# Kernel optimization log

Measured on AMD Instinct MI355X. Metric: run time of the kernel, lower is better.

## Reference

```python
import jax, jax.numpy as jnp
import numpy as np
import math

N_WAY, K_SHOT, Q_QUERY, PRJ_NUM, D = 5, 5, 15, 6, 64


def setup_inputs() -> dict:
    key = jax.random.key(0)
    k1, k2 = jax.random.split(key)
    feat = jax.random.normal(k1, (600, 64, 10, 10), dtype=jnp.float32)
    label = jax.random.randint(k2, (450,), 0, N_WAY)
    scale = jnp.ones((1,), dtype=jnp.float32)
    r = jnp.zeros((2,), dtype=jnp.float32)
    return {"feat": feat, "label": label, "scale": scale, "r": r}


def reference(feat, label, scale, r):
    ns = N_WAY * K_SHOT * PRJ_NUM  # 150 support images
    inv_sqrt_d = 1.0 / math.sqrt(D)
    support_xf = feat[:ns] * inv_sqrt_d
    query_xf = feat[ns:] * inv_sqrt_d
    q, c, h, w = query_xf.shape

    # support: (n_way, k_shot*prj_num*h*w, c)
    support = support_xf.reshape(N_WAY, K_SHOT * PRJ_NUM, c, h * w)
    support = jnp.transpose(support, (0, 1, 3, 2)).reshape(N_WAY, -1, c)
    # query: (q*h*w, c)
    query = jnp.transpose(query_xf.reshape(q, c, h * w), (0, 2, 1)).reshape(q * h * w, c)

    alpha, beta = r[0], r[1]
    reg = support.shape[1] / support.shape[2]
    lam = reg * jnp.exp(alpha)
    rho = jnp.exp(beta)

    # Woodbury / normal-equations path: hat = (S^T S + lam I)^-1 S^T S, per class
    sts = jnp.einsum('nkc,nkd->ncd', support, support)  # (n_way, c, c)
    m = sts + lam * jnp.eye(c, dtype=sts.dtype)[None]
    hat = jnp.linalg.inv(m) @ sts  # (n_way, c, c)

    Q_bar = jnp.einsum('qc,ncd->nqd', query, hat) * rho  # (n_way, q*h*w, c)
    dist = jnp.sum((Q_bar - query[None]) ** 2, axis=2).T  # (q*h*w, n_way)
    neg_l2_dist = -dist.reshape(q, h * w, N_WAY).mean(axis=1)  # (q, n_way)

    y_pred = jax.nn.softmax(neg_l2_dist, axis=1)
    logits = neg_l2_dist * scale[0]
    logp = jax.nn.log_softmax(logits, axis=1)
    loss = -jnp.mean(jnp.take_along_axis(logp, label[:, None], axis=1))
    return y_pred, loss
```

## Files before the change

kernel.cpp:

```cpp
#include <hip/hip_runtime.h>
#include <math.h>


typedef __attribute__((ext_vector_type(8))) short short8;
typedef __attribute__((ext_vector_type(4))) short short4v;
typedef __attribute__((ext_vector_type(4))) float f32x4;

#define NSUP 150
#define NQ 450
#define PIX 100
#define IMG_STRIDE 6400
#define MAGIC 0x5F3D2B1Cu

static __device__ __forceinline__ short bf16r(float x) {
  unsigned u = __builtin_bit_cast(unsigned, x);
  u += 0x7FFFu + ((u >> 16) & 1u);
  return (short)(u >> 16);
}
static __device__ __forceinline__ float b2f(short v) {
  return __builtin_bit_cast(float, ((unsigned)(unsigned short)v) << 16);
}
static __device__ __forceinline__ void st_flag(unsigned* p, unsigned v) {
  __threadfence();
  __hip_atomic_store(p, v, __ATOMIC_RELEASE, __HIP_MEMORY_SCOPE_AGENT);
}
static __device__ __forceinline__ void spin_flag(unsigned* p) {
  int guard = 1 << 22;
  while (__hip_atomic_load(p, __ATOMIC_ACQUIRE, __HIP_MEMORY_SCOPE_AGENT) != MAGIC
         && --guard) __builtin_amdgcn_s_sleep(2);
}

static __device__ __forceinline__ void gram_accum(const float* __restrict__ f,
                                                  f32x4 acc[4][4], int r, int g) {
  #pragma unroll
  for (int ks = 0; ks < 4; ++ks) {
    short8 frag[4];
    const int kb = ks * 32 + g * 8;
    #pragma unroll
    for (int R = 0; R < 4; ++R) {
      short8 q;
      const float* p = f + (R * 16 + r) * PIX + kb;
      if (ks < 3) {
        float4 lo = *(const float4*)p;
        float4 hi = *(const float4*)(p + 4);
        q[0] = bf16r(lo.x); q[1] = bf16r(lo.y); q[2] = bf16r(lo.z); q[3] = bf16r(lo.w);
        q[4] = bf16r(hi.x); q[5] = bf16r(hi.y); q[6] = bf16r(hi.z); q[7] = bf16r(hi.w);
      } else if (g == 0) {
        float4 lo = *(const float4*)p;
        q[0] = bf16r(lo.x); q[1] = bf16r(lo.y); q[2] = bf16r(lo.z); q[3] = bf16r(lo.w);
        q[4] = 0; q[5] = 0; q[6] = 0; q[7] = 0;
      } else {
        #pragma unroll
        for (int j = 0; j < 8; ++j) q[j] = 0;
      }
      frag[R] = q;
    }
    #pragma unroll
    for (int R = 0; R < 4; ++R)
      #pragma unroll
      for (int C = 0; C < 4; ++C)
        acc[R][C] = __builtin_amdgcn_mfma_f32_16x16x32_bf16(frag[R], frag[C],
                                                            acc[R][C], 0, 0, 0);
  }
}

static __device__ __forceinline__ void mm64q(const short* A, const short* B,
                                             f32x4 t[2][2], int r, int g,
                                             int wr, int wc) {
  #pragma unroll
  for (int ks = 0; ks < 2; ++ks) {
    short8 af[2], bfr[2];
    #pragma unroll
    for (int i = 0; i < 2; ++i) {
      af[i]  = *(const short8*)(A + (wr * 32 + i * 16 + r) * 72 + ks * 32 + g * 8);
      bfr[i] = *(const short8*)(B + (wc * 32 + i * 16 + r) * 72 + ks * 32 + g * 8);
    }
    #pragma unroll
    for (int i = 0; i < 2; ++i)
      #pragma unroll
      for (int j = 0; j < 2; ++j)
        t[i][j] = __builtin_amdgcn_mfma_f32_16x16x32_bf16(af[i], bfr[j],
                                                          t[i][j], 0, 0, 0);
  }
}

#define ZERO_ACC4(t)                                  \
  _Pragma("unroll") for (int R = 0; R < 4; ++R)       \
  _Pragma("unroll") for (int C = 0; C < 4; ++C)       \
  _Pragma("unroll") for (int q = 0; q < 4; ++q) t[R][C][q] = 0.f;

#define ZERO_ACC2(t)                                  \
  _Pragma("unroll") for (int R = 0; R < 2; ++R)       \
  _Pragma("unroll") for (int C = 0; C < 2; ++C)       \
  _Pragma("unroll") for (int q = 0; q < 4; ++q) t[R][C][q] = 0.f;

__global__ __launch_bounds__(256) void k_fused(
    const float* __restrict__ feat, const int* __restrict__ label,
    const float* __restrict__ scale, const float* __restrict__ rvec,
    float* __restrict__ out,
    float* __restrict__ partial,
    unsigned short* __restrict__ Gneg,
    float* __restrict__ blockloss,
    unsigned* __restrict__ gflag,
    unsigned* __restrict__ sflag,
    unsigned* __restrict__ lflag) {
  __shared__ __align__(16) char smem[65536];
  const int b = blockIdx.x, tid = threadIdx.x;
  const int wave = tid >> 6, lane = tid & 63;
  const int r = lane & 15, g = lane >> 4;

  if (b < 30) {
    float (*gbuf)[4096] = (float (*)[4096])smem;
    const int cls = b / 6, jb = b % 6;
    const int ks = wave, kb = ks * 32 + g * 8;
    f32x4 acc[4][4];
    ZERO_ACC4(acc)
    for (int im = 0; im < 5; ++im) {
      const float* f = feat + (size_t)(cls * 30 + jb * 5 + im) * IMG_STRIDE;
      short8 frag[4];
      #pragma unroll
      for (int R = 0; R < 4; ++R) {
        short8 q;
        const float* p = f + (R * 16 + r) * PIX + kb;
        if (ks < 3) {
          float4 lo = *(const float4*)p;
          float4 hi = *(const float4*)(p + 4);
          q[0] = bf16r(lo.x); q[1] = bf16r(lo.y); q[2] = bf16r(lo.z); q[3] = bf16r(lo.w);
          q[4] = bf16r(hi.x); q[5] = bf16r(hi.y); q[6] = bf16r(hi.z); q[7] = bf16r(hi.w);
        } else if (g == 0) {
          float4 lo = *(const float4*)p;
          q[0] = bf16r(lo.x); q[1] = bf16r(lo.y); q[2] = bf16r(lo.z); q[3] = bf16r(lo.w);
          q[4] = 0; q[5] = 0; q[6] = 0; q[7] = 0;
        } else {
          #pragma unroll
          for (int j = 0; j < 8; ++j) q[j] = 0;
        }
        frag[R] = q;
      }
      #pragma unroll
      for (int R = 0; R < 4; ++R)
        #pragma unroll
        for (int C = 0; C < 4; ++C)
          acc[R][C] = __builtin_amdgcn_mfma_f32_16x16x32_bf16(frag[R], frag[C],
                                                              acc[R][C], 0, 0, 0);
    }
    #pragma unroll
    for (int R = 0; R < 4; ++R)
      #pragma unroll
      for (int C = 0; C < 4; ++C)
        #pragma unroll
        for (int q = 0; q < 4; ++q) {
          const int row = R * 16 + g * 4 + q, col = C * 16 + r;
          gbuf[wave][row * 64 + col] = acc[R][C][q];
        }
    __syncthreads();
    float* outp = partial + (size_t)b * 4096;
    for (int c = tid; c < 1024; c += 256) {
      f32x4 s0 = *(const f32x4*)&gbuf[0][4 * c];
      f32x4 s1 = *(const f32x4*)&gbuf[1][4 * c];
      f32x4 s2 = *(const f32x4*)&gbuf[2][4 * c];
      f32x4 s3 = *(const f32x4*)&gbuf[3][4 * c];
      f32x4 s = s0 + s1 + s2 + s3;
      *(float4*)(outp + 4 * c) = *(float4*)&s;
    }
    __syncthreads();
    if (tid == 0) st_flag(&gflag[b], MAGIC);
    if (b >= 5) return;

    float* Ms   = (float*)(smem);
    short* Mb   = (short*)(smem + 16640);
    short* Tb   = (short*)(smem + 25856);
    short* Xa   = (short*)(smem + 35072);
    short* Xc   = (short*)(smem + 44288);
    float* radp = (float*)(smem + 53504);
    float* scal = (float*)(smem + 54528);

    const int n = b;
    const int wr = wave >> 1, wc = wave & 1;
    const float lam = 46.875f * expf(rvec[0]);
    const float rho = expf(rvec[1]);

    if (tid == 0)
      for (int i = 0; i < 6; ++i) spin_flag(&gflag[6 * n + i]);
    __syncthreads();

    {
      const float* base = partial + (size_t)n * 6 * 4096;
      for (int c = tid; c < 1024; c += 256) {
        float4 s = {0.f, 0.f, 0.f, 0.f};
        #pragma unroll
        for (int p = 0; p < 6; ++p) {
          float4 v = *(const float4*)(base + p * 4096 + 4 * c);
          s.x += v.x; s.y += v.y; s.z += v.z; s.w += v.w;
        }
        const int e = 4 * c, row = e >> 6, col = e & 63;
        Ms[row * 65 + col + 0] = s.x * (1.f / 64.f);
        Ms[row * 65 + col + 1] = s.y * (1.f / 64.f);
        Ms[row * 65 + col + 2] = s.z * (1.f / 64.f);
        Ms[row * 65 + col + 3] = s.w * (1.f / 64.f);
      }
    }
    __syncthreads();
    if (tid < 64) Ms[tid * 65 + tid] += lam;
    __syncthreads();

    {
      const int row = tid & 63, part = tid >> 6;
      float s = 0.f;
      #pragma unroll
      for (int k = 0; k < 16; ++k) s += fabsf(Ms[row * 65 + part * 16 + k]);
      radp[part * 64 + row] = s;
    }
    __syncthreads();
    if (tid < 64) {
      const float diag = Ms[tid * 65 + tid];
      const float rad = radp[tid] + radp[64 + tid] + radp[128 + tid] +
                        radp[192 + tid] - fabsf(diag);
      float lo = diag - rad, hi = diag + rad;
      for (int off = 32; off; off >>= 1) {
        lo = fminf(lo, __shfl_down(lo, off));
        hi = fmaxf(hi, __shfl_down(hi, off));
      }
      if (tid == 0) {
        const float a = fmaxf(lo, lam);
        const float bb = hi;
        const float s = a + bb, d = bb - a;
        scal[0] = s;
        scal[1] = 8.f / (2.f * s * s - d * d);
      }
    }
    __syncthreads();
    const float s0 = scal[0], theta = scal[1];

    for (int e = tid; e < 4096; e += 256) {
      const int i = e >> 6, j = e & 63;
      const float m = Ms[i * 65 + j];
      Mb[i * 72 + j] = bf16r(m);
      Xa[i * 72 + j] = bf16r(theta * (((i == j) ? s0 : 0.f) - m));
    }
    __syncthreads();

    short* x = Xa;
    short* xn = Xc;
    for (int it = 0; it < 2; ++it) {
      {
        f32x4 t[2][2];
        ZERO_ACC2(t)
        mm64q(x, Mb, t, r, g, wr, wc);
        #pragma unroll
        for (int i = 0; i < 2; ++i)
          #pragma unroll
          for (int j = 0; j < 2; ++j)
            #pragma unroll
            for (int q = 0; q < 4; ++q) {
              const int row = wr * 32 + i * 16 + g * 4 + q;
              const int col = wc * 32 + j * 16 + r;
              Tb[row * 72 + col] = bf16r(t[i][j][q]);
            }
      }
      __syncthreads();
      {
        f32x4 t[2][2];
        ZERO_ACC2(t)
        mm64q(Tb, x, t, r, g, wr, wc);
        #pragma unroll
        for (int i = 0; i < 2; ++i)
          #pragma unroll
          for (int j = 0; j < 2; ++j)
            #pragma unroll
            for (int q = 0; q < 4; ++q) {
              const int row = wr * 32 + i * 16 + g * 4 + q;
              const int col = wc * 32 + j * 16 + r;
              const int idx = row * 72 + col;
              xn[idx] = bf16r(2.f * b2f(x[idx]) - t[i][j][q]);
            }
      }
      __syncthreads();
      short* tmp = x; x = xn; xn = tmp;
    }

    for (int e = tid; e < 4096; e += 256) {
      const int i = e >> 6, j = e & 63;
      const float xv = b2f(x[i * 72 + j]);
      Tb[i * 72 + j] = bf16r(((i == j) ? (rho - 1.f) : 0.f) - rho * lam * xv);
    }
    __syncthreads();

    {
      f32x4 t[2][2];
      ZERO_ACC2(t)
      mm64q(Tb, Tb, t, r, g, wr, wc);
      #pragma unroll
      for (int i = 0; i < 2; ++i)
        #pragma unroll
        for (int j = 0; j < 2; ++j)
          #pragma unroll
          for (int q = 0; q < 4; ++q) {
            const int row = wr * 32 + i * 16 + g * 4 + q;
            const int col = wc * 32 + j * 16 + r;
            Gneg[n * 4096 + row * 64 + col] =
                (unsigned short)bf16r(t[i][j][q] * (-0.01f));
          }
    }
    __syncthreads();
    if (tid == 0) st_flag(&sflag[n], MAGIC);
    return;
  }

  const int img = (b - 30) * 4 + wave;
  const bool ok = img < NQ;
  f32x4 acc[4][4];
  ZERO_ACC4(acc)
  if (ok)
    gram_accum(feat + (size_t)(NSUP + img) * IMG_STRIDE, acc, r, g);

  if (tid == 0)
    for (int i = 0; i < 5; ++i) spin_flag(&sflag[i]);
  __syncthreads();

  unsigned short* Gs = (unsigned short*)smem;
  for (int e = tid; e < 5120; e += 256) {
    const int e4 = e * 4;
    const int nn = e4 >> 12, rem = e4 & 4095, row = rem >> 6, col = rem & 63;
    *(short4v*)&Gs[nn * 4352 + row * 68 + col] = *(const short4v*)&Gneg[e4];
  }
  __syncthreads();

  float myloss = 0.f;
  float nl[5] = {0.f, 0.f, 0.f, 0.f, 0.f};
  if (ok) {
    #pragma unroll
    for (int R = 0; R < 4; ++R)
      #pragma unroll
      for (int C = 0; C < 4; ++C)
        #pragma unroll
        for (int q = 0; q < 4; ++q) {
          const int row = R * 16 + g * 4 + q, col = C * 16 + r;
          const float cv = acc[R][C][q] * (1.f / 64.f);
          const int idx = row * 68 + col;
          #pragma unroll
          for (int nn = 0; nn < 5; ++nn)
            nl[nn] += b2f((short)Gs[nn * 4352 + idx]) * cv;
        }
    #pragma unroll
    for (int nn = 0; nn < 5; ++nn)
      for (int off = 32; off; off >>= 1) nl[nn] += __shfl_down(nl[nn], off);

    if (lane == 0) {
      float mx = nl[0];
      #pragma unroll
      for (int nn = 1; nn < 5; ++nn) mx = fmaxf(mx, nl[nn]);
      float ex[5], se = 0.f;
      #pragma unroll
      for (int nn = 0; nn < 5; ++nn) { ex[nn] = expf(nl[nn] - mx); se += ex[nn]; }
      const float inv = 1.f / se;
      #pragma unroll
      for (int nn = 0; nn < 5; ++nn) out[img * 5 + nn] = ex[nn] * inv;

      const float sc = scale[0];
      float mx2 = nl[0] * sc;
      #pragma unroll
      for (int nn = 1; nn < 5; ++nn) mx2 = fmaxf(mx2, nl[nn] * sc);
      float se2 = 0.f;
      #pragma unroll
      for (int nn = 0; nn < 5; ++nn) se2 += expf(nl[nn] * sc - mx2);
      myloss = mx2 + logf(se2) - nl[label[img]] * sc;
    }
  }

  float* wl = (float*)(smem + 43584);
  if (lane == 0) wl[wave] = ok ? myloss : 0.f;
  __syncthreads();
  if (tid == 0) {
    blockloss[b - 30] = wl[0] + wl[1] + wl[2] + wl[3];
    st_flag(&lflag[b - 30], MAGIC);
  }

  if (b == 30 && wave == 0) {
    for (int i = lane; i < 113; i += 64) spin_flag(&lflag[i]);
    float s = 0.f;
    for (int i = lane; i < 113; i += 64) s += blockloss[i];
    for (int off = 32; off; off >>= 1) s += __shfl_down(s, off);
    if (lane == 0) out[2250] = s / 450.f;
  }
}

extern "C" void kernel_launch(void* const* d_in, const int* in_sizes, int n_in,
                              void* d_out, int out_size, void* d_ws, size_t ws_size,
                              hipStream_t stream) {
  const float* feat  = (const float*)d_in[0];
  const int*   label = (const int*)d_in[1];
  const float* scale = (const float*)d_in[2];
  const float* rvec  = (const float*)d_in[3];
  float* out = (float*)d_out;

  char* ws = (char*)d_ws;
  float*          partial   = (float*)ws;
  unsigned short* Gneg      = (unsigned short*)(ws + 491520);
  float*          blockloss = (float*)(ws + 532480);
  unsigned*       flags     = (unsigned*)(ws + 532992);
  unsigned* gflag = flags;
  unsigned* sflag = flags + 32;
  unsigned* lflag = flags + 64;

  k_fused<<<dim3(143), dim3(256), 0, stream>>>(feat, label, scale, rvec, out,
                                               partial, Gneg, blockloss,
                                               gflag, sflag, lflag);
}
```

Baseline: 26.39 us.

## Widen grid and stage images into LDS via global_load_lds for Gram blocks

Support Gram computation is split across 75 blocks of two images each instead of 30 blocks of five, and the solve moves to its own 5 blocks. Each query image now gets two waves that split the K dimension and reduce partial Grams through shared memory. Images are staged into LDS with async global_load_lds, and the Gneg copy uses wider vectors with a padded stride. The goal is to spread the memory-bound Gram work over more CUs and shorten per-block latency. In exchange there are more partial Grams to reduce, more flags to spin on, and a longer final loss reduction across 225 blocks.

```diff
diff --git a/kernel.cpp b/kernel.cpp
--- a/kernel.cpp
+++ b/kernel.cpp
@@ -3,7 +3,6 @@
 
 
 typedef __attribute__((ext_vector_type(8))) short short8;
-typedef __attribute__((ext_vector_type(4))) short short4v;
 typedef __attribute__((ext_vector_type(4))) float f32x4;
 
 #define NSUP 150
@@ -30,38 +29,42 @@
          && --guard) __builtin_amdgcn_s_sleep(2);
 }
 
-static __device__ __forceinline__ void gram_accum(const float* __restrict__ f,
-                                                  f32x4 acc[4][4], int r, int g) {
+typedef const __attribute__((address_space(1))) void gas_void;
+typedef __attribute__((address_space(3))) void las_void;
+static __device__ __forceinline__ void gload1k(const float* src, float* dst, int lane) {
+  __builtin_amdgcn_global_load_lds((gas_void*)(src + lane * 4), (las_void*)dst,
+                                   16, 0, 0);
+}
+
+static __device__ __forceinline__ void gram_ks_lds(const float* img, f32x4 acc[4][4],
+                                                   int ks, int r, int g) {
+  short8 frag[4];
+  const int kb = ks * 32 + g * 8;
   #pragma unroll
-  for (int ks = 0; ks < 4; ++ks) {
-    short8 frag[4];
-    const int kb = ks * 32 + g * 8;
-    #pragma unroll
-    for (int R = 0; R < 4; ++R) {
-      short8 q;
-      const float* p = f + (R * 16 + r) * PIX + kb;
-      if (ks < 3) {
-        float4 lo = *(const float4*)p;
-        float4 hi = *(const float4*)(p + 4);
-        q[0] = bf16r(lo.x); q[1] = bf16r(lo.y); q[2] = bf16r(lo.z); q[3] = bf16r(lo.w);
-        q[4] = bf16r(hi.x); q[5] = bf16r(hi.y); q[6] = bf16r(hi.z); q[7] = bf16r(hi.w);
-      } else if (g == 0) {
-        float4 lo = *(const float4*)p;
-        q[0] = bf16r(lo.x); q[1] = bf16r(lo.y); q[2] = bf16r(lo.z); q[3] = bf16r(lo.w);
-        q[4] = 0; q[5] = 0; q[6] = 0; q[7] = 0;
-      } else {
-        #pragma unroll
-        for (int j = 0; j < 8; ++j) q[j] = 0;
-      }
-      frag[R] = q;
-    }
-    #pragma unroll
-    for (int R = 0; R < 4; ++R)
-      #pragma unroll
-      for (int C = 0; C < 4; ++C)
-        acc[R][C] = __builtin_amdgcn_mfma_f32_16x16x32_bf16(frag[R], frag[C],
-                                                            acc[R][C], 0, 0, 0);
-  }
+  for (int R = 0; R < 4; ++R) {
+    short8 q;
+    const float* p = img + (R * 16 + r) * PIX + kb;
+    if (ks < 3) {
+      float4 lo = *(const float4*)p;
+      float4 hi = *(const float4*)(p + 4);
+      q[0] = bf16r(lo.x); q[1] = bf16r(lo.y); q[2] = bf16r(lo.z); q[3] = bf16r(lo.w);
+      q[4] = bf16r(hi.x); q[5] = bf16r(hi.y); q[6] = bf16r(hi.z); q[7] = bf16r(hi.w);
+    } else if (g == 0) {
+      float4 lo = *(const float4*)p;
+      q[0] = bf16r(lo.x); q[1] = bf16r(lo.y); q[2] = bf16r(lo.z); q[3] = bf16r(lo.w);
+      q[4] = 0; q[5] = 0; q[6] = 0; q[7] = 0;
+    } else {
+      #pragma unroll
+      for (int j = 0; j < 8; ++j) q[j] = 0;
+    }
+    frag[R] = q;
+  }
+  #pragma unroll
+  for (int R = 0; R < 4; ++R)
+    #pragma unroll
+    for (int C = 0; C < 4; ++C)
+      acc[R][C] = __builtin_amdgcn_mfma_f32_16x16x32_bf16(frag[R], frag[C],
+                                                          acc[R][C], 0, 0, 0);
 }
 
 static __device__ __forceinline__ void mm64q(const short* A, const short* B,
@@ -109,41 +112,33 @@
   const int wave = tid >> 6, lane = tid & 63;
   const int r = lane & 15, g = lane >> 4;
 
-  if (b < 30) {
+  if (b < 75) {
+    float* img0 = (float*)smem;
+    float* img1 = (float*)(smem + 25600);
     float (*gbuf)[4096] = (float (*)[4096])smem;
-    const int cls = b / 6, jb = b % 6;
-    const int ks = wave, kb = ks * 32 + g * 8;
+    const int cls = b / 15, grp = b % 15;
+    const float* f0 = feat + (size_t)(cls * 30 + grp * 2) * IMG_STRIDE;
+    const float* f1 = f0 + IMG_STRIDE;
+
+    {
+      const int beg = (wave < 2) ? wave * 13 : 26 + (wave - 2) * 12;
+      const int cnt = (wave < 2) ? 13 : 12;
+      for (int i = 0; i < cnt; ++i) {
+        const int ch = beg + i;
+        const float* src = (ch < 25) ? f0 + ch * 256 : f1 + (ch - 25) * 256;
+        float* dst = (ch < 25) ? img0 + ch * 256 : img1 + (ch - 25) * 256;
+        gload1k(src, dst, lane);
+      }
+    }
+    asm volatile("s_waitcnt vmcnt(0)" ::: "memory");
+    __syncthreads();
+
     f32x4 acc[4][4];
     ZERO_ACC4(acc)
-    for (int im = 0; im < 5; ++im) {
-      const float* f = feat + (size_t)(cls * 30 + jb * 5 + im) * IMG_STRIDE;
-      short8 frag[4];
-      #pragma unroll
-      for (int R = 0; R < 4; ++R) {
-        short8 q;
-        const float* p = f + (R * 16 + r) * PIX + kb;
-        if (ks < 3) {
-          float4 lo = *(const float4*)p;
-          float4 hi = *(const float4*)(p + 4);
-          q[0] = bf16r(lo.x); q[1] = bf16r(lo.y); q[2] = bf16r(lo.z); q[3] = bf16r(lo.w);
-          q[4] = bf16r(hi.x); q[5] = bf16r(hi.y); q[6] = bf16r(hi.z); q[7] = bf16r(hi.w);
-        } else if (g == 0) {
-          float4 lo = *(const float4*)p;
-          q[0] = bf16r(lo.x); q[1] = bf16r(lo.y); q[2] = bf16r(lo.z); q[3] = bf16r(lo.w);
-          q[4] = 0; q[5] = 0; q[6] = 0; q[7] = 0;
-        } else {
-          #pragma unroll
-          for (int j = 0; j < 8; ++j) q[j] = 0;
-        }
-        frag[R] = q;
-      }
-      #pragma unroll
-      for (int R = 0; R < 4; ++R)
-        #pragma unroll
-        for (int C = 0; C < 4; ++C)
-          acc[R][C] = __builtin_amdgcn_mfma_f32_16x16x32_bf16(frag[R], frag[C],
-                                                              acc[R][C], 0, 0, 0);
-    }
+    gram_ks_lds(img0, acc, wave, r, g);
+    gram_ks_lds(img1, acc, wave, r, g);
+    __syncthreads();
+
     #pragma unroll
     for (int R = 0; R < 4; ++R)
       #pragma unroll
@@ -154,6 +149,7 @@
           gbuf[wave][row * 64 + col] = acc[R][C][q];
         }
     __syncthreads();
+
     float* outp = partial + (size_t)b * 4096;
     for (int c = tid; c < 1024; c += 256) {
       f32x4 s0 = *(const f32x4*)&gbuf[0][4 * c];
@@ -165,8 +161,10 @@
     }
     __syncthreads();
     if (tid == 0) st_flag(&gflag[b], MAGIC);
-    if (b >= 5) return;
-
+    return;
+  }
+
+  if (b < 80) {
     float* Ms   = (float*)(smem);
     short* Mb   = (short*)(smem + 16640);
     short* Tb   = (short*)(smem + 25856);
@@ -175,21 +173,20 @@
     float* radp = (float*)(smem + 53504);
     float* scal = (float*)(smem + 54528);
 
-    const int n = b;
+    const int n = b - 75;
     const int wr = wave >> 1, wc = wave & 1;
     const float lam = 46.875f * expf(rvec[0]);
     const float rho = expf(rvec[1]);
 
-    if (tid == 0)
-      for (int i = 0; i < 6; ++i) spin_flag(&gflag[6 * n + i]);
+    if (tid < 15) spin_flag(&gflag[n * 15 + tid]);
     __syncthreads();
 
     {
-      const float* base = partial + (size_t)n * 6 * 4096;
+      const float* base = partial + (size_t)n * 15 * 4096;
       for (int c = tid; c < 1024; c += 256) {
         float4 s = {0.f, 0.f, 0.f, 0.f};
         #pragma unroll
-        for (int p = 0; p < 6; ++p) {
+        for (int p = 0; p < 15; ++p) {
           float4 v = *(const float4*)(base + p * 4096 + 4 * c);
           s.x += v.x; s.y += v.y; s.z += v.z; s.w += v.w;
         }
@@ -307,28 +304,73 @@
     return;
   }
 
-  const int img = (b - 30) * 4 + wave;
-  const bool ok = img < NQ;
+  const int qb = b - 80;
+  float* imgA = (float*)smem;
+  float* imgB = (float*)(smem + 25600);
+  const int half = wave >> 1;
+  const int gimg = qb * 2 + half;
+  const float* fq = feat + (size_t)(NSUP + gimg) * IMG_STRIDE;
+  float* mybuf = half ? imgB : imgA;
+
+  {
+    const int w2 = wave & 1;
+    const int beg = w2 ? 13 : 0;
+    const int cnt = w2 ? 12 : 13;
+    for (int i = 0; i < cnt; ++i)
+      gload1k(fq + (beg + i) * 256, mybuf + (beg + i) * 256, lane);
+  }
+  asm volatile("s_waitcnt vmcnt(0)" ::: "memory");
+  __syncthreads();
+
   f32x4 acc[4][4];
   ZERO_ACC4(acc)
-  if (ok)
-    gram_accum(feat + (size_t)(NSUP + img) * IMG_STRIDE, acc, r, g);
-
-  if (tid == 0)
-    for (int i = 0; i < 5; ++i) spin_flag(&sflag[i]);
+  const int kbase = (wave & 1) * 2;
+  gram_ks_lds(mybuf, acc, kbase, r, g);
+  gram_ks_lds(mybuf, acc, kbase + 1, r, g);
+  __syncthreads();
+
+  float* p1 = (float*)(smem + 32768);
+  float* p3 = (float*)(smem + 49152);
+  if (wave & 1) {
+    float* dst = (wave == 1) ? p1 : p3;
+    #pragma unroll
+    for (int R = 0; R < 4; ++R)
+      #pragma unroll
+      for (int C = 0; C < 4; ++C)
+        #pragma unroll
+        for (int q = 0; q < 4; ++q) {
+          const int row = R * 16 + g * 4 + q, col = C * 16 + r;
+          dst[row * 64 + col] = acc[R][C][q];
+        }
+  }
+  __syncthreads();
+  if (!(wave & 1)) {
+    const float* src = (wave == 0) ? p1 : p3;
+    #pragma unroll
+    for (int R = 0; R < 4; ++R)
+      #pragma unroll
+      for (int C = 0; C < 4; ++C)
+        #pragma unroll
+        for (int q = 0; q < 4; ++q) {
+          const int row = R * 16 + g * 4 + q, col = C * 16 + r;
+          acc[R][C][q] += src[row * 64 + col];
+        }
+  }
+
+  if (tid < 5) spin_flag(&sflag[tid]);
   __syncthreads();
 
   unsigned short* Gs = (unsigned short*)smem;
-  for (int e = tid; e < 5120; e += 256) {
-    const int e4 = e * 4;
-    const int nn = e4 >> 12, rem = e4 & 4095, row = rem >> 6, col = rem & 63;
-    *(short4v*)&Gs[nn * 4352 + row * 68 + col] = *(const short4v*)&Gneg[e4];
-  }
-  __syncthreads();
-
-  float myloss = 0.f;
-  float nl[5] = {0.f, 0.f, 0.f, 0.f, 0.f};
-  if (ok) {
+  for (int e = tid; e < 2560; e += 256) {
+    const int nn = e >> 9, rem = e & 511, row = rem >> 3, c8 = (rem & 7) << 3;
+    *(short8*)&Gs[nn * 4608 + row * 72 + c8] =
+        *(const short8*)&Gneg[nn * 4096 + row * 64 + c8];
+  }
+  __syncthreads();
+
+  float* wl = (float*)(smem + 46080);
+  if (!(wave & 1)) {
+    float nl[5] = {0.f, 0.f, 0.f, 0.f, 0.f};
     #pragma unroll
     for (int R = 0; R < 4; ++R)
       #pragma unroll
@@ -337,10 +379,10 @@
         for (int q = 0; q < 4; ++q) {
           const int row = R * 16 + g * 4 + q, col = C * 16 + r;
           const float cv = acc[R][C][q] * (1.f / 64.f);
-          const int idx = row * 68 + col;
+          const int idx = row * 72 + col;
           #pragma unroll
           for (int nn = 0; nn < 5; ++nn)
-            nl[nn] += b2f((short)Gs[nn * 4352 + idx]) * cv;
+            nl[nn] += b2f((short)Gs[nn * 4608 + idx]) * cv;
         }
     #pragma unroll
     for (int nn = 0; nn < 5; ++nn)
@@ -355,7 +397,7 @@
       for (int nn = 0; nn < 5; ++nn) { ex[nn] = expf(nl[nn] - mx); se += ex[nn]; }
       const float inv = 1.f / se;
       #pragma unroll
-      for (int nn = 0; nn < 5; ++nn) out[img * 5 + nn] = ex[nn] * inv;
+      for (int nn = 0; nn < 5; ++nn) out[gimg * 5 + nn] = ex[nn] * inv;
 
       const float sc = scale[0];
       float mx2 = nl[0] * sc;
@@ -364,22 +406,19 @@
       float se2 = 0.f;
       #pragma unroll
       for (int nn = 0; nn < 5; ++nn) se2 += expf(nl[nn] * sc - mx2);
-      myloss = mx2 + logf(se2) - nl[label[img]] * sc;
-    }
-  }
-
-  float* wl = (float*)(smem + 43584);
-  if (lane == 0) wl[wave] = ok ? myloss : 0.f;
+      wl[half] = mx2 + logf(se2) - nl[label[gimg]] * sc;
+    }
+  }
   __syncthreads();
   if (tid == 0) {
-    blockloss[b - 30] = wl[0] + wl[1] + wl[2] + wl[3];
-    st_flag(&lflag[b - 30], MAGIC);
-  }
-
-  if (b == 30 && wave == 0) {
-    for (int i = lane; i < 113; i += 64) spin_flag(&lflag[i]);
+    blockloss[qb] = wl[0] + wl[1];
+    st_flag(&lflag[qb], MAGIC);
+  }
+
+  if (qb == 0 && wave == 0) {
+    for (int i = lane; i < 225; i += 64) spin_flag(&lflag[i]);
     float s = 0.f;
-    for (int i = lane; i < 113; i += 64) s += blockloss[i];
+    for (int i = lane; i < 225; i += 64) s += blockloss[i];
     for (int off = 32; off; off >>= 1) s += __shfl_down(s, off);
     if (lane == 0) out[2250] = s / 450.f;
   }
@@ -396,14 +435,14 @@
 
   char* ws = (char*)d_ws;
   float*          partial   = (float*)ws;
-  unsigned short* Gneg      = (unsigned short*)(ws + 491520);
-  float*          blockloss = (float*)(ws + 532480);
-  unsigned*       flags     = (unsigned*)(ws + 532992);
+  unsigned short* Gneg      = (unsigned short*)(ws + 1228800);
+  float*          blockloss = (float*)(ws + 1269760);
+  unsigned*       flags     = (unsigned*)(ws + 1270784);
   unsigned* gflag = flags;
-  unsigned* sflag = flags + 32;
-  unsigned* lflag = flags + 64;
-
-  k_fused<<<dim3(143), dim3(256), 0, stream>>>(feat, label, scale, rvec, out,
+  unsigned* sflag = flags + 80;
+  unsigned* lflag = flags + 96;
+
+  k_fused<<<dim3(305), dim3(256), 0, stream>>>(feat, label, scale, rvec, out,
                                                partial, Gneg, blockloss,
                                                gflag, sflag, lflag);
 }
```

New measurement: 28.33 us. +7.4%, slower.
